# Kernel optimization log

Hardware: AMD Instinct MI355X
Metric: run time of the kernel (lower is better)

Reference implementation:

```python
import jax, jax.numpy as jnp
import numpy as np

K_FRAC = 0.1      # module init: k (fraction of d)
SIGMA = 0.05      # module init: sigma


def setup_inputs() -> dict:
    key = jax.random.key(0)
    kx, kn = jax.random.split(key)
    b, num_samples, d = 32, 250, 1024
    x = jax.random.normal(kx, (b, d), dtype=jnp.float32)
    # replaces torch.normal(mean=0, std=1, size=(b, num_samples, d)) drawn inside forward
    noise = jax.random.normal(kn, (b, num_samples, d), dtype=jnp.float32)
    return {"x": x, "noise": noise}


def reference(x, noise):
    b, d = x.shape
    n = noise.shape[1]
    k = int(d * K_FRAC)
    k = max(1, min(k, d))  # clamp as in the torch code (train_mode=True path)

    # (b, n, d) perturbed scores
    perturbed = x[:, None, :] + noise * SIGMA

    # per-sample top-k indices; sort restores ascending index order as in torch.sort
    _, idx = jax.lax.top_k(perturbed, k)          # (b, n, k)
    idx = jnp.sort(idx, axis=-1)                  # (b, n, k)

    # one_hot(idx, d).mean(dim=1) == scatter-add of 1/n into (b, k, d)
    # (avoids materializing the (b, n, k, d) one-hot tensor)
    bb = jnp.arange(b)[:, None, None]             # (b, 1, 1)
    kk = jnp.arange(k)[None, None, :]             # (1, 1, k)
    indicators = jnp.zeros((b, k, d), dtype=x.dtype).at[bb, kk, idx].add(
        jnp.asarray(1.0 / n, dtype=x.dtype)
    )
    return indicators
```

## Files before the change

kernel.cpp:

```cpp
#include <hip/hip_runtime.h>


#define D_DIM 1024
#define K_SEL 102
#define K_PAD 104
#define RPB 4
#define SIGMA 0.05f
#define WAVES_PER_BLOCK 4
#define BLOCK (WAVES_PER_BLOCK * 64)
#define SLOTS 16

__device__ __forceinline__ unsigned int float_to_key(float f) {
    unsigned int u = __float_as_uint(f);
    return (u & 0x80000000u) ? ~u : (u | 0x80000000u);
}

__device__ __forceinline__ unsigned int wave_incl_scan(unsigned int v) {
    v += (unsigned int)__builtin_amdgcn_update_dpp(0, (int)v, 0x111, 0xF, 0xF, false);
    v += (unsigned int)__builtin_amdgcn_update_dpp(0, (int)v, 0x112, 0xF, 0xF, false);
    v += (unsigned int)__builtin_amdgcn_update_dpp(0, (int)v, 0x114, 0xF, 0xF, false);
    v += (unsigned int)__builtin_amdgcn_update_dpp(0, (int)v, 0x118, 0xF, 0xF, false);
    v += (unsigned int)__builtin_amdgcn_update_dpp(0, (int)v, 0x142, 0xA, 0xF, false);
    v += (unsigned int)__builtin_amdgcn_update_dpp(0, (int)v, 0x143, 0xC, 0xF, false);
    return v;
}
__device__ __forceinline__ unsigned int wave_sum_u32(unsigned int v) {
    return (unsigned int)__builtin_amdgcn_readlane((int)wave_incl_scan(v), 63);
}

__device__ __forceinline__ unsigned int count_ge2(const unsigned int* key,
                                                  unsigned int m1, unsigned int m2) {
    unsigned int a = 0, b = 0;
    #pragma unroll
    for (int j = 0; j < SLOTS; ++j) {
        a += (key[j] >= m1) ? 1u : 0u;
        b += (key[j] >= m2) ? 1u : 0u;
    }
    return wave_sum_u32(a | (b << 16));
}

template <bool USE_WS>
__global__ __launch_bounds__(BLOCK)
void ptopk_select(const float* __restrict__ x,
                  const float* __restrict__ noise,
                  unsigned short* __restrict__ ws_idx,
                  float* __restrict__ out,
                  int n_samples, float inv_n, int nrows) {
    const int wid  = threadIdx.x >> 6;
    const int lane = threadIdx.x & 63;
    const int row  = blockIdx.x * WAVES_PER_BLOCK + wid;
    if (row >= nrows) return;
    const int bb = row / n_samples;
    const int ss = row - bb * n_samples;

    const float4* nrow =
        reinterpret_cast<const float4*>(noise + (size_t)row * D_DIM + lane * SLOTS);
    const float4* xrow =
        reinterpret_cast<const float4*>(x + (size_t)bb * D_DIM + lane * SLOTS);

    unsigned int key[SLOTS];
    #pragma unroll
    for (int c = 0; c < 4; ++c) {
        const float4 nv = nrow[c];
        const float4 xv = xrow[c];
        key[c*4+0] = float_to_key(fmaf(nv.x, SIGMA, xv.x));
        key[c*4+1] = float_to_key(fmaf(nv.y, SIGMA, xv.y));
        key[c*4+2] = float_to_key(fmaf(nv.z, SIGMA, xv.z));
        key[c*4+3] = float_to_key(fmaf(nv.w, SIGMA, xv.w));
    }

    const unsigned int B1 = float_to_key(1.07f);
    const unsigned int B2 = float_to_key(1.17f);
    const unsigned int B3 = float_to_key(1.25f);
    const unsigned int B4 = float_to_key(1.32f);
    const unsigned int B5 = float_to_key(1.40f);
    const unsigned int B6 = float_to_key(1.50f);
    unsigned int pA = 0, pB = 0, pC = 0;
    #pragma unroll
    for (int j = 0; j < SLOTS; ++j) {
        pA += ((key[j] >= B1) ? 1u : 0u) + ((key[j] >= B2) ? 0x10000u : 0u);
        pB += ((key[j] >= B3) ? 1u : 0u) + ((key[j] >= B4) ? 0x10000u : 0u);
        pC += ((key[j] >= B5) ? 1u : 0u) + ((key[j] >= B6) ? 0x10000u : 0u);
    }
    const unsigned int tA = wave_sum_u32(pA);
    const unsigned int tB = wave_sum_u32(pB);
    const unsigned int tC = wave_sum_u32(pC);
    const unsigned int c1 = tA & 0xFFFFu, c2 = tA >> 16;
    const unsigned int c3 = tB & 0xFFFFu, c4 = tB >> 16;
    const unsigned int c5 = tC & 0xFFFFu, c6 = tC >> 16;

    unsigned int lo, hi, c_lo, c_hi;
    if (c6 >= K_SEL)      { lo = B6; c_lo = c6;    hi = 0xFFFFFFFFu; c_hi = 0u; }
    else if (c5 >= K_SEL) { lo = B5; c_lo = c5;    hi = B6; c_hi = c6; }
    else if (c4 >= K_SEL) { lo = B4; c_lo = c4;    hi = B5; c_hi = c5; }
    else if (c3 >= K_SEL) { lo = B3; c_lo = c3;    hi = B4; c_hi = c4; }
    else if (c2 >= K_SEL) { lo = B2; c_lo = c2;    hi = B3; c_hi = c3; }
    else if (c1 >= K_SEL) { lo = B1; c_lo = c1;    hi = B2; c_hi = c2; }
    else                  { lo = 0u; c_lo = D_DIM; hi = B1; c_hi = c1; }

    while (c_lo != K_SEL && (hi - lo) > 1u) {
        const unsigned int span = hi - lo;
        unsigned int o1 = (unsigned int)((float)(c_lo - K_SEL) * (float)span /
                                         (float)(c_lo - c_hi));
        unsigned int o2 = span >> 1;
        if (o1 < 1u) o1 = 1u;
        if (o1 > span - 1u) o1 = span - 1u;
        const unsigned int mA = lo + (o1 < o2 ? o1 : o2);
        const unsigned int mB = lo + (o1 < o2 ? o2 : o1);

        const unsigned int s = count_ge2(key, mA, mB);
        const unsigned int cA = s & 0xFFFFu;
        const unsigned int cB = s >> 16;

        if (cB >= K_SEL)      { lo = mB; c_lo = cB; }
        else if (cA >= K_SEL) { lo = mA; c_lo = cA; hi = mB; c_hi = cB; }
        else                  { hi = mA; c_hi = cA; }
    }

    unsigned int SEL_B, kkf, tieK;
    if (c_lo == K_SEL) { SEL_B = lo; kkf = 0u;           tieK = 0u; }
    else               { SEL_B = hi; kkf = K_SEL - c_hi; tieK = lo; }

    unsigned int sel = 0u, alive = 0u;
    #pragma unroll
    for (int j = 0; j < SLOTS; ++j) {
        sel   |= (key[j] >= SEL_B) ? (1u << j) : 0u;
        alive |= (key[j] == tieK)  ? (1u << j) : 0u;
    }

    const unsigned int mine =
        ((unsigned int)__popc(sel) << 16) | (unsigned int)__popc(alive);
    unsigned int run = wave_incl_scan(mine) - mine;

    unsigned short* wb = ws_idx + ((size_t)bb * n_samples + ss) * K_PAD;
    float* orow = out + (size_t)bb * (K_SEL * D_DIM);
    const int base_i = lane * SLOTS;
    unsigned int both = sel | alive;
    while (both) {
        const int j = __builtin_ctz(both);
        both &= both - 1u;
        const unsigned int gtp = run >> 16;
        const unsigned int eqp = run & 0xFFFFu;
        if (sel & (1u << j)) {
            const unsigned int rank = gtp + (eqp < kkf ? eqp : kkf);
            if (USE_WS) wb[rank] = (unsigned short)(base_i + j);
            else atomicAdd(orow + (size_t)rank * D_DIM + (base_i + j), inv_n);
            run += 0x10000u;
        } else {
            if (eqp < kkf) {
                if (USE_WS) wb[gtp + eqp] = (unsigned short)(base_i + j);
                else atomicAdd(orow + (size_t)(gtp + eqp) * D_DIM + (base_i + j), inv_n);
            }
            run += 1u;
        }
    }
}

__global__ __launch_bounds__(256)
void ptopk_hist(const unsigned short* __restrict__ ws_idx,
                float* __restrict__ out,
                int n_samples, float inv_n) {
    __shared__ unsigned int cnt[RPB][D_DIM];
    const int tid  = threadIdx.x;
    const int ngrp = K_PAD / RPB;
    const int b_   = blockIdx.x / ngrp;
    const int g_   = blockIdx.x - b_ * ngrp;
    const int r0   = g_ * RPB;

    uint4* cz = reinterpret_cast<uint4*>(&cnt[0][0]);
    #pragma unroll
    for (int c = 0; c < (RPB * D_DIM) / (4 * 256); ++c)
        cz[c * 256 + tid] = make_uint4(0u, 0u, 0u, 0u);
    __syncthreads();

    for (int s = tid; s < n_samples; s += 256) {
        const unsigned long long v = *reinterpret_cast<const unsigned long long*>(
            ws_idx + ((size_t)b_ * n_samples + s) * K_PAD + r0);
        #pragma unroll
        for (int e = 0; e < RPB; ++e) {
            const unsigned int idx = (unsigned int)((v >> (16 * e)) & 0xFFFFu) & (D_DIM - 1u);
            atomicAdd(&cnt[e][idx], 1u);
        }
    }
    __syncthreads();

    const int i = tid * 4;
    #pragma unroll
    for (int e = 0; e < RPB; ++e) {
        const int rank = r0 + e;
        if (rank < K_SEL) {
            float4* dst = reinterpret_cast<float4*>(out + ((size_t)b_ * K_SEL + rank) * D_DIM);
            dst[tid] = make_float4(cnt[e][i] * inv_n, cnt[e][i + 1] * inv_n,
                                   cnt[e][i + 2] * inv_n, cnt[e][i + 3] * inv_n);
        }
    }
}

__global__ __launch_bounds__(256)
void zero_kernel(float4* __restrict__ p, int n4) {
    const int i = blockIdx.x * 256 + threadIdx.x;
    if (i < n4) p[i] = make_float4(0.f, 0.f, 0.f, 0.f);
}

extern "C" void kernel_launch(void* const* d_in, const int* in_sizes, int n_in,
                              void* d_out, int out_size, void* d_ws, size_t ws_size,
                              hipStream_t stream) {
    const float* x     = (const float*)d_in[0];
    const float* noise = (const float*)d_in[1];
    float* out = (float*)d_out;

    const int d = D_DIM;
    const int b = in_sizes[0] / d;
    const int n = in_sizes[1] / in_sizes[0];
    const int rows = b * n;
    const float inv_n = 1.0f / (float)n;
    const int grid = (rows + WAVES_PER_BLOCK - 1) / WAVES_PER_BLOCK;

    const size_t ws_needed = (size_t)b * n * K_PAD * sizeof(unsigned short);
    if (ws_size >= ws_needed) {
        unsigned short* ws_idx = (unsigned short*)d_ws;
        ptopk_select<true><<<grid, BLOCK, 0, stream>>>(x, noise, ws_idx, out,
                                                       n, inv_n, rows);
        ptopk_hist<<<b * (K_PAD / RPB), 256, 0, stream>>>(ws_idx, out, n, inv_n);
    } else {
        const int n4 = out_size / 4;
        zero_kernel<<<(n4 + 255) / 256, 256, 0, stream>>>((float4*)out, n4);
        ptopk_select<false><<<grid, BLOCK, 0, stream>>>(x, noise, nullptr, out,
                                                        n, inv_n, rows);
    }
}
```

Measured before the change: 26.26 us.

## Interleave row elements across lanes and rank selections with ballot/mbcnt

Each lane now owns elements lane + 64*j (strided) instead of a contiguous block of 16, so global loads become coalesced scalar loads across the wave. Selected indices are ranked per slot with ballot plus mbcnt instead of a wave-wide DPP prefix scan followed by a divergent per-lane ctz loop. A fast path skips tie handling when the threshold picks exactly k elements. The trade-off is sixteen dword loads per lane instead of four float4 loads, and more ballot instructions per row.

```diff
diff --git a/kernel.cpp b/kernel.cpp
--- a/kernel.cpp
+++ b/kernel.cpp
@@ -15,17 +15,19 @@
     return (u & 0x80000000u) ? ~u : (u | 0x80000000u);
 }
 
-__device__ __forceinline__ unsigned int wave_incl_scan(unsigned int v) {
+__device__ __forceinline__ unsigned int mbcnt64(unsigned long long m) {
+    return __builtin_amdgcn_mbcnt_hi((unsigned int)(m >> 32),
+           __builtin_amdgcn_mbcnt_lo((unsigned int)m, 0u));
+}
+
+__device__ __forceinline__ unsigned int wave_sum_u32(unsigned int v) {
     v += (unsigned int)__builtin_amdgcn_update_dpp(0, (int)v, 0x111, 0xF, 0xF, false);
     v += (unsigned int)__builtin_amdgcn_update_dpp(0, (int)v, 0x112, 0xF, 0xF, false);
     v += (unsigned int)__builtin_amdgcn_update_dpp(0, (int)v, 0x114, 0xF, 0xF, false);
     v += (unsigned int)__builtin_amdgcn_update_dpp(0, (int)v, 0x118, 0xF, 0xF, false);
     v += (unsigned int)__builtin_amdgcn_update_dpp(0, (int)v, 0x142, 0xA, 0xF, false);
     v += (unsigned int)__builtin_amdgcn_update_dpp(0, (int)v, 0x143, 0xC, 0xF, false);
-    return v;
-}
-__device__ __forceinline__ unsigned int wave_sum_u32(unsigned int v) {
-    return (unsigned int)__builtin_amdgcn_readlane((int)wave_incl_scan(v), 63);
+    return (unsigned int)__builtin_amdgcn_readlane((int)v, 63);
 }
 
 __device__ __forceinline__ unsigned int count_ge2(const unsigned int* key,
@@ -53,21 +55,13 @@
     const int bb = row / n_samples;
     const int ss = row - bb * n_samples;
 
-    const float4* nrow =
-        reinterpret_cast<const float4*>(noise + (size_t)row * D_DIM + lane * SLOTS);
-    const float4* xrow =
-        reinterpret_cast<const float4*>(x + (size_t)bb * D_DIM + lane * SLOTS);
+    const float* nbase = noise + (size_t)row * D_DIM + lane;
+    const float* xbase = x + (size_t)bb * D_DIM + lane;
 
     unsigned int key[SLOTS];
     #pragma unroll
-    for (int c = 0; c < 4; ++c) {
-        const float4 nv = nrow[c];
-        const float4 xv = xrow[c];
-        key[c*4+0] = float_to_key(fmaf(nv.x, SIGMA, xv.x));
-        key[c*4+1] = float_to_key(fmaf(nv.y, SIGMA, xv.y));
-        key[c*4+2] = float_to_key(fmaf(nv.z, SIGMA, xv.z));
-        key[c*4+3] = float_to_key(fmaf(nv.w, SIGMA, xv.w));
-    }
+    for (int j = 0; j < SLOTS; ++j)
+        key[j] = float_to_key(fmaf(nbase[j * 64], SIGMA, xbase[j * 64]));
 
     const unsigned int B1 = float_to_key(1.07f);
     const unsigned int B2 = float_to_key(1.17f);
@@ -121,37 +115,44 @@
     if (c_lo == K_SEL) { SEL_B = lo; kkf = 0u;           tieK = 0u; }
     else               { SEL_B = hi; kkf = K_SEL - c_hi; tieK = lo; }
 
-    unsigned int sel = 0u, alive = 0u;
-    #pragma unroll
-    for (int j = 0; j < SLOTS; ++j) {
-        sel   |= (key[j] >= SEL_B) ? (1u << j) : 0u;
-        alive |= (key[j] == tieK)  ? (1u << j) : 0u;
-    }
-
-    const unsigned int mine =
-        ((unsigned int)__popc(sel) << 16) | (unsigned int)__popc(alive);
-    unsigned int run = wave_incl_scan(mine) - mine;
-
     unsigned short* wb = ws_idx + ((size_t)bb * n_samples + ss) * K_PAD;
     float* orow = out + (size_t)bb * (K_SEL * D_DIM);
-    const int base_i = lane * SLOTS;
-    unsigned int both = sel | alive;
-    while (both) {
-        const int j = __builtin_ctz(both);
-        both &= both - 1u;
-        const unsigned int gtp = run >> 16;
-        const unsigned int eqp = run & 0xFFFFu;
-        if (sel & (1u << j)) {
-            const unsigned int rank = gtp + (eqp < kkf ? eqp : kkf);
-            if (USE_WS) wb[rank] = (unsigned short)(base_i + j);
-            else atomicAdd(orow + (size_t)rank * D_DIM + (base_i + j), inv_n);
-            run += 0x10000u;
-        } else {
-            if (eqp < kkf) {
-                if (USE_WS) wb[gtp + eqp] = (unsigned short)(base_i + j);
-                else atomicAdd(orow + (size_t)(gtp + eqp) * D_DIM + (base_i + j), inv_n);
+
+    if (kkf == 0u) {
+        unsigned int base = 0u;
+        #pragma unroll
+        for (int j = 0; j < SLOTS; ++j) {
+            const bool p = key[j] >= SEL_B;
+            const unsigned long long sb = __ballot(p);
+            if (p) {
+                const unsigned int rank = base + mbcnt64(sb);
+                const unsigned int idx  = (unsigned int)(j * 64) + lane;
+                if (USE_WS) wb[rank] = (unsigned short)idx;
+                else atomicAdd(orow + (size_t)rank * D_DIM + idx, inv_n);
             }
-            run += 1u;
+            base += (unsigned int)__popcll(sb);
+        }
+    } else {
+        unsigned int gt_base = 0u, eq_base = 0u;
+        #pragma unroll
+        for (int j = 0; j < SLOTS; ++j) {
+            const bool pg = key[j] >= SEL_B;
+            const bool pe = key[j] == tieK;
+            const unsigned long long sb = __ballot(pg);
+            const unsigned long long ab = __ballot(pe);
+            const unsigned int gtp = gt_base + mbcnt64(sb);
+            const unsigned int eqp = eq_base + mbcnt64(ab);
+            const unsigned int idx = (unsigned int)(j * 64) + lane;
+            if (pg) {
+                const unsigned int rank = gtp + (eqp < kkf ? eqp : kkf);
+                if (USE_WS) wb[rank] = (unsigned short)idx;
+                else atomicAdd(orow + (size_t)rank * D_DIM + idx, inv_n);
+            } else if (pe && eqp < kkf) {
+                if (USE_WS) wb[gtp + eqp] = (unsigned short)idx;
+                else atomicAdd(orow + (size_t)(gtp + eqp) * D_DIM + idx, inv_n);
+            }
+            gt_base += (unsigned int)__popcll(sb);
+            eq_base += (unsigned int)__popcll(ab);
         }
     }
 }
```

Measured after the change: 26.78 us. Within noise of the previous version (+2.0%).
